# Optimization experiments

Hardware: AMD Instinct MI355X
Metric: run time of the kernel (lower is better)

The kernel has to match this reference:

```python
import jax, jax.numpy as jnp
import numpy as np

N = 100000   # nodes
E = 1600000  # edges (avg degree 16)
D = 64       # in_channels
OUT = 64     # out_channels


def setup_inputs() -> dict:
    key = jax.random.key(0)
    k1, k2, k3, k4, k5 = jax.random.split(key, 5)
    x = jax.random.normal(k1, (N, D), jnp.float32)
    edge_index = jax.random.randint(k2, (2, E), 0, N, dtype=jnp.int32)
    x0 = jax.random.normal(k3, (N, D), jnp.float32)
    W_weight = jax.random.normal(k4, (OUT, D), jnp.float32) * (1.0 / np.sqrt(D))
    W_bias = jax.random.normal(k5, (OUT,), jnp.float32) * 0.01
    return {"x": x, "edge_index": edge_index, "x0": x0,
            "W_weight": W_weight, "W_bias": W_bias}


def reference(x, edge_index, x0, W_bias, W_weight):
    n = x.shape[0]
    # gcn_norm with add_self_loops=True (PyG default), improved=False
    self_loops = jnp.arange(n, dtype=edge_index.dtype)
    row = jnp.concatenate([edge_index[0], self_loops])  # source nodes
    col = jnp.concatenate([edge_index[1], self_loops])  # target nodes
    w = jnp.ones(row.shape[0], dtype=x.dtype)
    deg = jax.ops.segment_sum(w, col, num_segments=n)   # in-degree (+1 self loop)
    deg_inv_sqrt = jnp.where(deg > 0, jax.lax.rsqrt(jnp.maximum(deg, 1e-12)), 0.0)
    norm = deg_inv_sqrt[row] * deg_inv_sqrt[col]        # [E+N]
    # SpMM: adj_t = SparseTensor(row=col, col=row) -> out[c] = sum_e norm_e * x[row_e]
    agg = jax.ops.segment_sum(x[row] * norm[:, None], col, num_segments=n)  # [N, D]
    # use_init=False, use_weight=True -> trailing Linear
    return agg @ W_weight.T + W_bias
```

## Files before the change

### kernel.cpp

```cpp
#include <hip/hip_runtime.h>


#define NBMAX 400
#define CAP   5120

typedef short bf16x8 __attribute__((ext_vector_type(8)));
typedef float f32x4  __attribute__((ext_vector_type(4)));

__device__ inline float bflo(unsigned u) { return __uint_as_float(u << 16); }
__device__ inline float bfhi(unsigned u) { return __uint_as_float(u & 0xFFFF0000u); }
__device__ inline unsigned short f2bf(float f) {
    unsigned u = __float_as_uint(f);
    u += 0x7FFFu + ((u >> 16) & 1u);
    return (unsigned short)(u >> 16);
}

__global__ __launch_bounds__(256) void k_bin(const int* __restrict__ row,
                                             const int* __restrict__ col,
                                             int* __restrict__ gcnt,
                                             unsigned int* __restrict__ ebuf, int E) {
    __shared__ unsigned int   sorted4[4096];
    __shared__ unsigned short sbkt[4096];
    __shared__ int h[NBMAX], hstart[NBMAX], hcur[NBMAX], gof[NBMAX];
    int t = threadIdx.x;
    int base = blockIdx.x * 4096;
    int total = min(4096, E - base);

    int rr[16], cc[16];
    #pragma unroll
    for (int i = 0; i < 4; ++i) {
        int e0 = (t + i * 256) * 4;
        if (e0 + 3 < total) {
            int4 r4 = *(const int4*)(row + base + e0);
            int4 c4 = *(const int4*)(col + base + e0);
            rr[i*4+0]=r4.x; rr[i*4+1]=r4.y; rr[i*4+2]=r4.z; rr[i*4+3]=r4.w;
            cc[i*4+0]=c4.x; cc[i*4+1]=c4.y; cc[i*4+2]=c4.z; cc[i*4+3]=c4.w;
        } else {
            #pragma unroll
            for (int j = 0; j < 4; ++j) {
                int e = e0 + j;
                if (e < total) { rr[i*4+j] = row[base+e]; cc[i*4+j] = col[base+e]; }
                else cc[i*4+j] = -1;
            }
        }
    }
    for (int b = t; b < NBMAX; b += 256) h[b] = 0;
    __syncthreads();
    #pragma unroll
    for (int i = 0; i < 16; ++i)
        if (cc[i] >= 0) atomicAdd(&h[cc[i] >> 8], 1);
    __syncthreads();
    if (t < 64) {
        int lo = t * 7;
        int loc[7]; int s = 0;
        #pragma unroll
        for (int i = 0; i < 7; ++i) {
            loc[i] = s;
            int idx = lo + i;
            s += (idx < NBMAX) ? h[idx] : 0;
        }
        int incl = s;
        for (int off = 1; off < 64; off <<= 1) {
            int v = __shfl_up(incl, off);
            if (t >= off) incl += v;
        }
        int ex = incl - s;
        #pragma unroll
        for (int i = 0; i < 7; ++i) {
            int idx = lo + i;
            if (idx < NBMAX) hstart[idx] = ex + loc[i];
        }
    }
    __syncthreads();
    for (int b = t; b < NBMAX; b += 256) hcur[b] = hstart[b];
    __syncthreads();
    #pragma unroll
    for (int i = 0; i < 16; ++i) {
        if (cc[i] >= 0) {
            int b = cc[i] >> 8;
            int rank = atomicAdd(&hcur[b], 1);
            sorted4[rank] = (unsigned)rr[i] | ((unsigned)(cc[i] & 255) << 24);
            sbkt[rank] = (unsigned short)b;
        }
    }
    for (int b = t; b < NBMAX; b += 256) {
        int m = h[b];
        gof[b] = b * CAP + (m ? atomicAdd(&gcnt[b], m) : 0);
    }
    __syncthreads();
    for (int i = t; i < total; i += 256) {
        int b = sbkt[i];
        ebuf[gof[b] + (i - hstart[b])] = sorted4[i];
    }
}

__global__ __launch_bounds__(256) void k_cnt(const unsigned int* __restrict__ ebuf,
                                             const int* __restrict__ gcnt,
                                             float* __restrict__ dinv, int n) {
    __shared__ int h[256];
    int b = blockIdx.x, t = threadIdx.x;
    int s0 = b * CAP;
    int count = min(gcnt[b], CAP);
    h[t] = 0;
    __syncthreads();
    for (int i = t; i < count; i += 256) atomicAdd(&h[ebuf[s0 + i] >> 24], 1);
    __syncthreads();
    int c = b * 256 + t;
    if (c < n) dinv[c] = rsqrtf((float)(h[t] + 1));
}

__global__ __launch_bounds__(256) void k_gemm(const float* __restrict__ x,
                                              const float* __restrict__ W,
                                              const float* __restrict__ dinv,
                                              unsigned short* __restrict__ yb, int n) {
    __shared__ __align__(16) unsigned short xs[64][72];
    __shared__ __align__(16) unsigned short Wb[64][72];
    __shared__ __align__(16) unsigned short ys[64][68];
    int t = threadIdx.x;
    long long total = (long long)n * 64;
    long long xbase = (long long)blockIdx.x * 4096;
    #pragma unroll
    for (int i = 0; i < 4; ++i) {
        int idx = t + i * 256;
        int r = idx >> 4, c4 = (idx & 15) << 2;
        long long g = xbase + (long long)idx * 4;
        float4 v;
        if (g + 3 < total) v = *(const float4*)(x + g);
        else {
            v.x = (g + 0 < total) ? x[g + 0] : 0.f;
            v.y = (g + 1 < total) ? x[g + 1] : 0.f;
            v.z = (g + 2 < total) ? x[g + 2] : 0.f;
            v.w = (g + 3 < total) ? x[g + 3] : 0.f;
        }
        ushort4 o; o.x = f2bf(v.x); o.y = f2bf(v.y); o.z = f2bf(v.z); o.w = f2bf(v.w);
        *(ushort4*)&xs[r][c4] = o;
        float4 wv = *(const float4*)(W + idx * 4);
        ushort4 wo; wo.x = f2bf(wv.x); wo.y = f2bf(wv.y); wo.z = f2bf(wv.z); wo.w = f2bf(wv.w);
        *(ushort4*)&Wb[r][c4] = wo;
    }
    __syncthreads();
    int lane = t & 63, wid = t >> 6;
    int m  = wid * 16 + (lane & 15);
    int kg = (lane >> 4) * 8;
    bf16x8 a0 = *(bf16x8*)&xs[m][kg];
    bf16x8 a1 = *(bf16x8*)&xs[m][32 + kg];
    int bn = lane & 15;
    f32x4 acc0 = {0.f,0.f,0.f,0.f}, acc1 = acc0, acc2 = acc0, acc3 = acc0;
    {
        bf16x8 b0 = *(bf16x8*)&Wb[bn][kg], b1 = *(bf16x8*)&Wb[bn][32 + kg];
        acc0 = __builtin_amdgcn_mfma_f32_16x16x32_bf16(a0, b0, acc0, 0, 0, 0);
        acc0 = __builtin_amdgcn_mfma_f32_16x16x32_bf16(a1, b1, acc0, 0, 0, 0);
    }
    {
        bf16x8 b0 = *(bf16x8*)&Wb[bn + 16][kg], b1 = *(bf16x8*)&Wb[bn + 16][32 + kg];
        acc1 = __builtin_amdgcn_mfma_f32_16x16x32_bf16(a0, b0, acc1, 0, 0, 0);
        acc1 = __builtin_amdgcn_mfma_f32_16x16x32_bf16(a1, b1, acc1, 0, 0, 0);
    }
    {
        bf16x8 b0 = *(bf16x8*)&Wb[bn + 32][kg], b1 = *(bf16x8*)&Wb[bn + 32][32 + kg];
        acc2 = __builtin_amdgcn_mfma_f32_16x16x32_bf16(a0, b0, acc2, 0, 0, 0);
        acc2 = __builtin_amdgcn_mfma_f32_16x16x32_bf16(a1, b1, acc2, 0, 0, 0);
    }
    {
        bf16x8 b0 = *(bf16x8*)&Wb[bn + 48][kg], b1 = *(bf16x8*)&Wb[bn + 48][32 + kg];
        acc3 = __builtin_amdgcn_mfma_f32_16x16x32_bf16(a0, b0, acc3, 0, 0, 0);
        acc3 = __builtin_amdgcn_mfma_f32_16x16x32_bf16(a1, b1, acc3, 0, 0, 0);
    }
    int lr0 = wid * 16 + (lane >> 4) * 4;
    int q = lane & 15;
    #pragma unroll
    for (int i = 0; i < 4; ++i) {
        int r = blockIdx.x * 64 + lr0 + i;
        float dv = (r < n) ? dinv[r] : 0.f;
        ys[lr0 + i][q +  0] = f2bf(dv * acc0[i]);
        ys[lr0 + i][q + 16] = f2bf(dv * acc1[i]);
        ys[lr0 + i][q + 32] = f2bf(dv * acc2[i]);
        ys[lr0 + i][q + 48] = f2bf(dv * acc3[i]);
    }
    __syncthreads();
    #pragma unroll
    for (int it = 0; it < 4; ++it) {
        int idx = t + it * 256;
        int rr2 = idx >> 4, c4 = (idx & 15) << 2;
        int r = blockIdx.x * 64 + rr2;
        if (r < n)
            *(ushort4*)&yb[(long long)r * 64 + c4] = *(ushort4*)&ys[rr2][c4];
    }
}

__global__ __launch_bounds__(1024) void k_aggr(const unsigned int* __restrict__ ebuf,
                                               const int* __restrict__ gcnt,
                                               const float* __restrict__ dinv,
                                               const unsigned short* __restrict__ yb,
                                               const float* __restrict__ bias,
                                               float* __restrict__ out, int n) {
    __shared__ int h[256], hstart[256], hc[256], wsum[4];
    __shared__ int sbuf[CAP];
    int b = blockIdx.x, t = threadIdx.x;
    int s0 = b * CAP;
    int count = min(gcnt[b], CAP);

    if (t < 256) h[t] = 0;
    __syncthreads();
    unsigned rec[5];
    #pragma unroll
    for (int k = 0; k < 5; ++k) {
        int i = t + k * 1024;
        if (i < count) {
            unsigned p = ebuf[s0 + i];
            rec[k] = p;
            atomicAdd(&h[p >> 24], 1);
        }
    }
    __syncthreads();
    if (t < 256) {
        int v = h[t];
        int lane = t & 63, wid = t >> 6;
        int incl = v;
        #pragma unroll
        for (int off = 1; off < 64; off <<= 1) {
            int u = __shfl_up(incl, off);
            if (lane >= off) incl += u;
        }
        hstart[t] = incl;
        if (lane == 63) wsum[wid] = incl;
    }
    __syncthreads();
    if (t < 256) {
        int wid = t >> 6;
        int add = 0;
        for (int w = 0; w < wid; ++w) add += wsum[w];
        int ex = hstart[t] - h[t] + add;
        hstart[t] = ex;
        hc[t] = ex;
    }
    __syncthreads();
    #pragma unroll
    for (int k = 0; k < 5; ++k) {
        int i = t + k * 1024;
        if (i < count) {
            unsigned p = rec[k];
            int r = atomicAdd(&hc[p >> 24], 1);
            sbuf[r] = (int)(p & 0x1FFFFu);
        }
    }
    __syncthreads();

    int lane = t & 63, w = t >> 6;
    int g = lane >> 4, q = lane & 15;
    #pragma unroll
    for (int r = 0; r < 4; ++r) {
        int cl = r * 64 + w * 4 + g;
        int c = b * 256 + cl;
        if (c >= n) continue;
        int start = hstart[cl], len = h[cl];
        float a0 = 0.f, a1 = 0.f, a2 = 0.f, a3 = 0.f;
        if (len > 0) {
            int sc = sbuf[start];
            for (int i = 0; i < len; ++i) {
                int sn = (i + 1 < len) ? sbuf[start + i + 1] : 0;
                float2 v = *(const float2*)(yb + (long long)sc * 64 + (q << 2));
                unsigned u0 = __float_as_uint(v.x), u1 = __float_as_uint(v.y);
                a0 += bflo(u0); a1 += bfhi(u0);
                a2 += bflo(u1); a3 += bfhi(u1);
                sc = sn;
            }
        }
        {
            float2 v = *(const float2*)(yb + (long long)c * 64 + (q << 2));
            unsigned u0 = __float_as_uint(v.x), u1 = __float_as_uint(v.y);
            a0 += bflo(u0); a1 += bfhi(u0);
            a2 += bflo(u1); a3 += bfhi(u1);
        }
        float dc = dinv[c];
        float4 bv = *(const float4*)(bias + (q << 2));
        *(float4*)(out + (long long)c * 64 + (q << 2)) =
            make_float4(dc * a0 + bv.x, dc * a1 + bv.y,
                        dc * a2 + bv.z, dc * a3 + bv.w);
    }
}

extern "C" void kernel_launch(void* const* d_in, const int* in_sizes, int n_in,
                              void* d_out, int out_size, void* d_ws, size_t ws_size,
                              hipStream_t stream) {
    const float* x    = (const float*)d_in[0];
    const int*   ei   = (const int*)d_in[1];
    const float* W    = (const float*)d_in[3];
    const float* bias = (const float*)d_in[4];
    float* out = (float*)d_out;

    int n = in_sizes[0] / 64;
    int E = in_sizes[1] / 2;
    const int* row = ei;
    const int* col = ei + E;

    int NB = (n + 255) / 256;

    char* ws = (char*)d_ws;
    size_t off = 0;
    auto alloc = [&](size_t bytes) { char* p = ws + off; off += (bytes + 15) & ~size_t(15); return p; };
    int*            gcnt = (int*)  alloc((size_t)NB * 4);
    float*          dinv = (float*)alloc((size_t)n * 4);
    unsigned short* yb   = (unsigned short*)alloc((size_t)n * 64 * 2);
    unsigned int*   ebuf = (unsigned int*)alloc((size_t)NB * CAP * 4);

    int nbE = (E + 4095) / 4096;

    hipMemsetAsync(gcnt, 0, (size_t)NB * 4, stream);
    k_bin <<<nbE, 256, 0, stream>>>(row, col, gcnt, ebuf, E);
    k_cnt <<<NB, 256, 0, stream>>>(ebuf, gcnt, dinv, n);
    k_gemm<<<(n + 63) / 64, 256, 0, stream>>>(x, W, dinv, yb, n);
    k_aggr<<<NB, 1024, 0, stream>>>(ebuf, gcnt, dinv, yb, bias, out, n);
}
```

Before: 182.1 us.

## Merge edge binning and GEMM into one launch, move source norm into aggregation

Edge binning and the dense X·W^T GEMM now run as disjoint block ranges of a single kernel, so the GEMM no longer has to wait for the degree count and the two stages can overlap. Because the GEMM no longer has dinv available, the source-side normalisation moves into the aggregation loop, which now loads dinv[src] per edge (prefetched one ahead) and also scales the self-loop term. The GEMM's yb output is written with scalar per-element stores instead of a coalesced staged write through shared memory. The cost is an extra random dinv gather per edge and less coalesced yb writes.

```diff
diff --git a/kernel.cpp b/kernel.cpp
--- a/kernel.cpp
+++ b/kernel.cpp
@@ -15,82 +15,158 @@
     return (unsigned short)(u >> 16);
 }
 
-__global__ __launch_bounds__(256) void k_bin(const int* __restrict__ row,
-                                             const int* __restrict__ col,
-                                             int* __restrict__ gcnt,
-                                             unsigned int* __restrict__ ebuf, int E) {
-    __shared__ unsigned int   sorted4[4096];
-    __shared__ unsigned short sbkt[4096];
-    __shared__ int h[NBMAX], hstart[NBMAX], hcur[NBMAX], gof[NBMAX];
+__global__ __launch_bounds__(256) void k_fused(const int* __restrict__ row,
+                                               const int* __restrict__ col,
+                                               int* __restrict__ gcnt,
+                                               unsigned int* __restrict__ ebuf, int E,
+                                               const float* __restrict__ x,
+                                               const float* __restrict__ W,
+                                               unsigned short* __restrict__ yb, int n,
+                                               int nbBin) {
+    __shared__ __align__(16) char smem[30976];
     int t = threadIdx.x;
-    int base = blockIdx.x * 4096;
-    int total = min(4096, E - base);
-
-    int rr[16], cc[16];
-    #pragma unroll
-    for (int i = 0; i < 4; ++i) {
-        int e0 = (t + i * 256) * 4;
-        if (e0 + 3 < total) {
-            int4 r4 = *(const int4*)(row + base + e0);
-            int4 c4 = *(const int4*)(col + base + e0);
-            rr[i*4+0]=r4.x; rr[i*4+1]=r4.y; rr[i*4+2]=r4.z; rr[i*4+3]=r4.w;
-            cc[i*4+0]=c4.x; cc[i*4+1]=c4.y; cc[i*4+2]=c4.z; cc[i*4+3]=c4.w;
-        } else {
+
+    if ((int)blockIdx.x < nbBin) {
+        unsigned int*   sorted4 = (unsigned int*)smem;
+        unsigned short* sbkt    = (unsigned short*)(smem + 16384);
+        int* h      = (int*)(smem + 24576);
+        int* hstart = (int*)(smem + 26176);
+        int* hcur   = (int*)(smem + 27776);
+        int* gof    = (int*)(smem + 29376);
+        int base = blockIdx.x * 4096;
+        int total = min(4096, E - base);
+
+        int rr[16], cc[16];
+        #pragma unroll
+        for (int i = 0; i < 4; ++i) {
+            int e0 = (t + i * 256) * 4;
+            if (e0 + 3 < total) {
+                int4 r4 = *(const int4*)(row + base + e0);
+                int4 c4 = *(const int4*)(col + base + e0);
+                rr[i*4+0]=r4.x; rr[i*4+1]=r4.y; rr[i*4+2]=r4.z; rr[i*4+3]=r4.w;
+                cc[i*4+0]=c4.x; cc[i*4+1]=c4.y; cc[i*4+2]=c4.z; cc[i*4+3]=c4.w;
+            } else {
+                #pragma unroll
+                for (int j = 0; j < 4; ++j) {
+                    int e = e0 + j;
+                    if (e < total) { rr[i*4+j] = row[base+e]; cc[i*4+j] = col[base+e]; }
+                    else cc[i*4+j] = -1;
+                }
+            }
+        }
+        for (int b = t; b < NBMAX; b += 256) h[b] = 0;
+        __syncthreads();
+        #pragma unroll
+        for (int i = 0; i < 16; ++i)
+            if (cc[i] >= 0) atomicAdd(&h[cc[i] >> 8], 1);
+        __syncthreads();
+        if (t < 64) {
+            int lo = t * 7;
+            int loc[7]; int s = 0;
             #pragma unroll
-            for (int j = 0; j < 4; ++j) {
-                int e = e0 + j;
-                if (e < total) { rr[i*4+j] = row[base+e]; cc[i*4+j] = col[base+e]; }
-                else cc[i*4+j] = -1;
-            }
-        }
-    }
-    for (int b = t; b < NBMAX; b += 256) h[b] = 0;
-    __syncthreads();
-    #pragma unroll
-    for (int i = 0; i < 16; ++i)
-        if (cc[i] >= 0) atomicAdd(&h[cc[i] >> 8], 1);
-    __syncthreads();
-    if (t < 64) {
-        int lo = t * 7;
-        int loc[7]; int s = 0;
-        #pragma unroll
-        for (int i = 0; i < 7; ++i) {
-            loc[i] = s;
-            int idx = lo + i;
-            s += (idx < NBMAX) ? h[idx] : 0;
-        }
-        int incl = s;
-        for (int off = 1; off < 64; off <<= 1) {
-            int v = __shfl_up(incl, off);
-            if (t >= off) incl += v;
-        }
-        int ex = incl - s;
-        #pragma unroll
-        for (int i = 0; i < 7; ++i) {
-            int idx = lo + i;
-            if (idx < NBMAX) hstart[idx] = ex + loc[i];
-        }
-    }
-    __syncthreads();
-    for (int b = t; b < NBMAX; b += 256) hcur[b] = hstart[b];
-    __syncthreads();
-    #pragma unroll
-    for (int i = 0; i < 16; ++i) {
-        if (cc[i] >= 0) {
-            int b = cc[i] >> 8;
-            int rank = atomicAdd(&hcur[b], 1);
-            sorted4[rank] = (unsigned)rr[i] | ((unsigned)(cc[i] & 255) << 24);
-            sbkt[rank] = (unsigned short)b;
-        }
-    }
-    for (int b = t; b < NBMAX; b += 256) {
-        int m = h[b];
-        gof[b] = b * CAP + (m ? atomicAdd(&gcnt[b], m) : 0);
-    }
-    __syncthreads();
-    for (int i = t; i < total; i += 256) {
-        int b = sbkt[i];
-        ebuf[gof[b] + (i - hstart[b])] = sorted4[i];
+            for (int i = 0; i < 7; ++i) {
+                loc[i] = s;
+                int idx = lo + i;
+                s += (idx < NBMAX) ? h[idx] : 0;
+            }
+            int incl = s;
+            for (int off = 1; off < 64; off <<= 1) {
+                int v = __shfl_up(incl, off);
+                if (t >= off) incl += v;
+            }
+            int ex = incl - s;
+            #pragma unroll
+            for (int i = 0; i < 7; ++i) {
+                int idx = lo + i;
+                if (idx < NBMAX) hstart[idx] = ex + loc[i];
+            }
+        }
+        __syncthreads();
+        for (int b = t; b < NBMAX; b += 256) hcur[b] = hstart[b];
+        __syncthreads();
+        #pragma unroll
+        for (int i = 0; i < 16; ++i) {
+            if (cc[i] >= 0) {
+                int b = cc[i] >> 8;
+                int rank = atomicAdd(&hcur[b], 1);
+                sorted4[rank] = (unsigned)rr[i] | ((unsigned)(cc[i] & 255) << 24);
+                sbkt[rank] = (unsigned short)b;
+            }
+        }
+        for (int b = t; b < NBMAX; b += 256) {
+            int m = h[b];
+            gof[b] = b * CAP + (m ? atomicAdd(&gcnt[b], m) : 0);
+        }
+        __syncthreads();
+        for (int i = t; i < total; i += 256) {
+            int b = sbkt[i];
+            ebuf[gof[b] + (i - hstart[b])] = sorted4[i];
+        }
+    } else {
+        unsigned short (*xs)[72] = (unsigned short (*)[72])smem;
+        unsigned short (*Wb)[72] = (unsigned short (*)[72])(smem + 9216);
+        int gb = blockIdx.x - nbBin;
+        long long total = (long long)n * 64;
+        long long xbase = (long long)gb * 4096;
+        #pragma unroll
+        for (int i = 0; i < 4; ++i) {
+            int idx = t + i * 256;
+            int r = idx >> 4, c4 = (idx & 15) << 2;
+            long long g = xbase + (long long)idx * 4;
+            float4 v;
+            if (g + 3 < total) v = *(const float4*)(x + g);
+            else {
+                v.x = (g + 0 < total) ? x[g + 0] : 0.f;
+                v.y = (g + 1 < total) ? x[g + 1] : 0.f;
+                v.z = (g + 2 < total) ? x[g + 2] : 0.f;
+                v.w = (g + 3 < total) ? x[g + 3] : 0.f;
+            }
+            ushort4 o; o.x = f2bf(v.x); o.y = f2bf(v.y); o.z = f2bf(v.z); o.w = f2bf(v.w);
+            *(ushort4*)&xs[r][c4] = o;
+            float4 wv = *(const float4*)(W + idx * 4);
+            ushort4 wo; wo.x = f2bf(wv.x); wo.y = f2bf(wv.y); wo.z = f2bf(wv.z); wo.w = f2bf(wv.w);
+            *(ushort4*)&Wb[r][c4] = wo;
+        }
+        __syncthreads();
+        int lane = t & 63, wid = t >> 6;
+        int m  = wid * 16 + (lane & 15);
+        int kg = (lane >> 4) * 8;
+        bf16x8 a0 = *(bf16x8*)&xs[m][kg];
+        bf16x8 a1 = *(bf16x8*)&xs[m][32 + kg];
+        int bn = lane & 15;
+        f32x4 acc0 = {0.f,0.f,0.f,0.f}, acc1 = acc0, acc2 = acc0, acc3 = acc0;
+        {
+            bf16x8 b0 = *(bf16x8*)&Wb[bn][kg], b1 = *(bf16x8*)&Wb[bn][32 + kg];
+            acc0 = __builtin_amdgcn_mfma_f32_16x16x32_bf16(a0, b0, acc0, 0, 0, 0);
+            acc0 = __builtin_amdgcn_mfma_f32_16x16x32_bf16(a1, b1, acc0, 0, 0, 0);
+        }
+        {
+            bf16x8 b0 = *(bf16x8*)&Wb[bn + 16][kg], b1 = *(bf16x8*)&Wb[bn + 16][32 + kg];
+            acc1 = __builtin_amdgcn_mfma_f32_16x16x32_bf16(a0, b0, acc1, 0, 0, 0);
+            acc1 = __builtin_amdgcn_mfma_f32_16x16x32_bf16(a1, b1, acc1, 0, 0, 0);
+        }
+        {
+            bf16x8 b0 = *(bf16x8*)&Wb[bn + 32][kg], b1 = *(bf16x8*)&Wb[bn + 32][32 + kg];
+            acc2 = __builtin_amdgcn_mfma_f32_16x16x32_bf16(a0, b0, acc2, 0, 0, 0);
+            acc2 = __builtin_amdgcn_mfma_f32_16x16x32_bf16(a1, b1, acc2, 0, 0, 0);
+        }
+        {
+            bf16x8 b0 = *(bf16x8*)&Wb[bn + 48][kg], b1 = *(bf16x8*)&Wb[bn + 48][32 + kg];
+            acc3 = __builtin_amdgcn_mfma_f32_16x16x32_bf16(a0, b0, acc3, 0, 0, 0);
+            acc3 = __builtin_amdgcn_mfma_f32_16x16x32_bf16(a1, b1, acc3, 0, 0, 0);
+        }
+        int rbase = gb * 64 + wid * 16 + (lane >> 4) * 4;
+        #pragma unroll
+        for (int i = 0; i < 4; ++i) {
+            int r = rbase + i;
+            if (r < n) {
+                long long ro = (long long)r * 64 + bn;
+                yb[ro +  0] = f2bf(acc0[i]);
+                yb[ro + 16] = f2bf(acc1[i]);
+                yb[ro + 32] = f2bf(acc2[i]);
+                yb[ro + 48] = f2bf(acc3[i]);
+            }
+        }
     }
 }
 
@@ -107,85 +183,6 @@
     __syncthreads();
     int c = b * 256 + t;
     if (c < n) dinv[c] = rsqrtf((float)(h[t] + 1));
-}
-
-__global__ __launch_bounds__(256) void k_gemm(const float* __restrict__ x,
-                                              const float* __restrict__ W,
-                                              const float* __restrict__ dinv,
-                                              unsigned short* __restrict__ yb, int n) {
-    __shared__ __align__(16) unsigned short xs[64][72];
-    __shared__ __align__(16) unsigned short Wb[64][72];
-    __shared__ __align__(16) unsigned short ys[64][68];
-    int t = threadIdx.x;
-    long long total = (long long)n * 64;
-    long long xbase = (long long)blockIdx.x * 4096;
-    #pragma unroll
-    for (int i = 0; i < 4; ++i) {
-        int idx = t + i * 256;
-        int r = idx >> 4, c4 = (idx & 15) << 2;
-        long long g = xbase + (long long)idx * 4;
-        float4 v;
-        if (g + 3 < total) v = *(const float4*)(x + g);
-        else {
-            v.x = (g + 0 < total) ? x[g + 0] : 0.f;
-            v.y = (g + 1 < total) ? x[g + 1] : 0.f;
-            v.z = (g + 2 < total) ? x[g + 2] : 0.f;
-            v.w = (g + 3 < total) ? x[g + 3] : 0.f;
-        }
-        ushort4 o; o.x = f2bf(v.x); o.y = f2bf(v.y); o.z = f2bf(v.z); o.w = f2bf(v.w);
-        *(ushort4*)&xs[r][c4] = o;
-        float4 wv = *(const float4*)(W + idx * 4);
-        ushort4 wo; wo.x = f2bf(wv.x); wo.y = f2bf(wv.y); wo.z = f2bf(wv.z); wo.w = f2bf(wv.w);
-        *(ushort4*)&Wb[r][c4] = wo;
-    }
-    __syncthreads();
-    int lane = t & 63, wid = t >> 6;
-    int m  = wid * 16 + (lane & 15);
-    int kg = (lane >> 4) * 8;
-    bf16x8 a0 = *(bf16x8*)&xs[m][kg];
-    bf16x8 a1 = *(bf16x8*)&xs[m][32 + kg];
-    int bn = lane & 15;
-    f32x4 acc0 = {0.f,0.f,0.f,0.f}, acc1 = acc0, acc2 = acc0, acc3 = acc0;
-    {
-        bf16x8 b0 = *(bf16x8*)&Wb[bn][kg], b1 = *(bf16x8*)&Wb[bn][32 + kg];
-        acc0 = __builtin_amdgcn_mfma_f32_16x16x32_bf16(a0, b0, acc0, 0, 0, 0);
-        acc0 = __builtin_amdgcn_mfma_f32_16x16x32_bf16(a1, b1, acc0, 0, 0, 0);
-    }
-    {
-        bf16x8 b0 = *(bf16x8*)&Wb[bn + 16][kg], b1 = *(bf16x8*)&Wb[bn + 16][32 + kg];
-        acc1 = __builtin_amdgcn_mfma_f32_16x16x32_bf16(a0, b0, acc1, 0, 0, 0);
-        acc1 = __builtin_amdgcn_mfma_f32_16x16x32_bf16(a1, b1, acc1, 0, 0, 0);
-    }
-    {
-        bf16x8 b0 = *(bf16x8*)&Wb[bn + 32][kg], b1 = *(bf16x8*)&Wb[bn + 32][32 + kg];
-        acc2 = __builtin_amdgcn_mfma_f32_16x16x32_bf16(a0, b0, acc2, 0, 0, 0);
-        acc2 = __builtin_amdgcn_mfma_f32_16x16x32_bf16(a1, b1, acc2, 0, 0, 0);
-    }
-    {
-        bf16x8 b0 = *(bf16x8*)&Wb[bn + 48][kg], b1 = *(bf16x8*)&Wb[bn + 48][32 + kg];
-        acc3 = __builtin_amdgcn_mfma_f32_16x16x32_bf16(a0, b0, acc3, 0, 0, 0);
-        acc3 = __builtin_amdgcn_mfma_f32_16x16x32_bf16(a1, b1, acc3, 0, 0, 0);
-    }
-    int lr0 = wid * 16 + (lane >> 4) * 4;
-    int q = lane & 15;
-    #pragma unroll
-    for (int i = 0; i < 4; ++i) {
-        int r = blockIdx.x * 64 + lr0 + i;
-        float dv = (r < n) ? dinv[r] : 0.f;
-        ys[lr0 + i][q +  0] = f2bf(dv * acc0[i]);
-        ys[lr0 + i][q + 16] = f2bf(dv * acc1[i]);
-        ys[lr0 + i][q + 32] = f2bf(dv * acc2[i]);
-        ys[lr0 + i][q + 48] = f2bf(dv * acc3[i]);
-    }
-    __syncthreads();
-    #pragma unroll
-    for (int it = 0; it < 4; ++it) {
-        int idx = t + it * 256;
-        int rr2 = idx >> 4, c4 = (idx & 15) << 2;
-        int r = blockIdx.x * 64 + rr2;
-        if (r < n)
-            *(ushort4*)&yb[(long long)r * 64 + c4] = *(ushort4*)&ys[rr2][c4];
-    }
 }
 
 __global__ __launch_bounds__(1024) void k_aggr(const unsigned int* __restrict__ ebuf,
@@ -257,22 +254,24 @@
         float a0 = 0.f, a1 = 0.f, a2 = 0.f, a3 = 0.f;
         if (len > 0) {
             int sc = sbuf[start];
+            float ds = dinv[sc];
             for (int i = 0; i < len; ++i) {
                 int sn = (i + 1 < len) ? sbuf[start + i + 1] : 0;
+                float dn = dinv[sn];
                 float2 v = *(const float2*)(yb + (long long)sc * 64 + (q << 2));
                 unsigned u0 = __float_as_uint(v.x), u1 = __float_as_uint(v.y);
-                a0 += bflo(u0); a1 += bfhi(u0);
-                a2 += bflo(u1); a3 += bfhi(u1);
-                sc = sn;
-            }
-        }
+                a0 += ds * bflo(u0); a1 += ds * bfhi(u0);
+                a2 += ds * bflo(u1); a3 += ds * bfhi(u1);
+                sc = sn; ds = dn;
+            }
+        }
+        float dc = dinv[c];
         {
             float2 v = *(const float2*)(yb + (long long)c * 64 + (q << 2));
             unsigned u0 = __float_as_uint(v.x), u1 = __float_as_uint(v.y);
-            a0 += bflo(u0); a1 += bfhi(u0);
-            a2 += bflo(u1); a3 += bfhi(u1);
-        }
-        float dc = dinv[c];
+            a0 += dc * bflo(u0); a1 += dc * bfhi(u0);
+            a2 += dc * bflo(u1); a3 += dc * bfhi(u1);
+        }
         float4 bv = *(const float4*)(bias + (q << 2));
         *(float4*)(out + (long long)c * 64 + (q << 2)) =
             make_float4(dc * a0 + bv.x, dc * a1 + bv.y,
@@ -304,11 +303,12 @@
     unsigned short* yb   = (unsigned short*)alloc((size_t)n * 64 * 2);
     unsigned int*   ebuf = (unsigned int*)alloc((size_t)NB * CAP * 4);
 
-    int nbE = (E + 4095) / 4096;
+    int nbBin  = (E + 4095) / 4096;
+    int nbGemm = (n + 63) / 64;
 
     hipMemsetAsync(gcnt, 0, (size_t)NB * 4, stream);
-    k_bin <<<nbE, 256, 0, stream>>>(row, col, gcnt, ebuf, E);
+    k_fused<<<nbBin + nbGemm, 256, 0, stream>>>(row, col, gcnt, ebuf, E,
+                                                x, W, yb, n, nbBin);
     k_cnt <<<NB, 256, 0, stream>>>(ebuf, gcnt, dinv, n);
-    k_gemm<<<(n + 63) / 64, 256, 0, stream>>>(x, W, dinv, yb, n);
     k_aggr<<<NB, 1024, 0, stream>>>(ebuf, gcnt, dinv, yb, bias, out, n);
 }
```

Measured after the change: 182.8 us. No clear change (+0.4%).
